# Performance work log

Hardware: AMD Instinct MI355X
Metric: run time of the kernel (lower is better)

## Reference

```python
import jax, jax.numpy as jnp
import numpy as np

B, T, D = 16, 2048, 1024


def setup_inputs() -> dict:
    key = jax.random.key(0)
    ks = jax.random.split(key, 7)
    s = 1.0 / np.sqrt(D)  # nn.Linear default init bound
    u = lambda k, shape: jax.random.uniform(k, shape, jnp.float32, -s, s)
    return {
        "x": jax.random.normal(ks[0], (B, T, D), jnp.float32),
        "h0": jnp.zeros((B, D), jnp.float32),
        "W_in": u(ks[1], (2 * D, D)),
        "b_in": u(ks[2], (2 * D,)),
        "W_dt": u(ks[3], (D, D)),
        "b_dt": u(ks[4], (D,)),
        "W_out": u(ks[5], (D, D)),
        "b_out": u(ks[6], (D,)),
    }


def reference(x, h0, W_in, b_in, W_dt, b_dt, W_out, b_out):
    # in_proj then chunk: first half x_part, second half gate
    xz = jnp.einsum("btd,ed->bte", x, W_in) + b_in          # [B,T,2D]
    x_part, gate = jnp.split(xz, 2, axis=-1)                  # each [B,T,D]
    dt = jax.nn.sigmoid(jnp.einsum("btd,ed->bte", x_part, W_dt) + b_dt)  # [B,T,D]

    def step(h, inp):
        dt_t, xp_t = inp                                      # [B,D] each
        h = (1.0 - dt_t) * h + dt_t * xp_t                    # gated EMA update
        return h, h

    _, hs = jax.lax.scan(step, h0,
                         (jnp.swapaxes(dt, 0, 1), jnp.swapaxes(x_part, 0, 1)))
    hs = jnp.swapaxes(hs, 0, 1)                               # [B,T,D]
    y = jnp.einsum("btd,ed->bte", hs * jax.nn.sigmoid(gate), W_out) + b_out
    return y
```

## Files before the change

### kernel.cpp

```cpp
#include <hip/hip_runtime.h>
#include <hip/hip_bf16.h>
#include <cstdint>

typedef __attribute__((ext_vector_type(8))) short short8;
typedef __attribute__((ext_vector_type(4))) float f32x4;
typedef __attribute__((ext_vector_type(8))) unsigned short ushort8;

#define B_ 16
#define T_ 2048
#define D_ 1024
#define M_ (B_*T_)
#define NC 32
#define CL 64

static __device__ __forceinline__ float bf2f(unsigned short u) {
  unsigned int x = ((unsigned int)u) << 16;
  return __builtin_bit_cast(float, x);
}
static __device__ __forceinline__ unsigned short f2bf(float f) {
  unsigned int x = __builtin_bit_cast(unsigned int, f);
  unsigned int r = x + 0x7fffu + ((x >> 16) & 1u);
  return (unsigned short)(r >> 16);
}
static __device__ __forceinline__ float sigmoidf(float v) {
  return 1.f / (1.f + __expf(-v));
}

typedef const __attribute__((address_space(1))) unsigned int* gas1_t;
typedef __attribute__((address_space(3))) unsigned int* las3_t;
static __device__ __forceinline__ void async_copy16(const void* g, void* l) {
  __builtin_amdgcn_global_load_lds((gas1_t)g, (las3_t)l, 16, 0, 0);
}

#define VMCNT4 asm volatile("s_waitcnt vmcnt(4)" ::: "memory")
#define VMCNT2 asm volatile("s_waitcnt vmcnt(2)" ::: "memory")
#define VMCNT0 asm volatile("s_waitcnt vmcnt(0)" ::: "memory")
#define LGKM0  asm volatile("s_waitcnt lgkmcnt(0)" ::: "memory")
#define SBAR   __builtin_amdgcn_s_barrier()
#define SCHED0 __builtin_amdgcn_sched_barrier(0)

__global__ void cvt_f32_bf16(const float* __restrict__ in,
                             unsigned short* __restrict__ out, long n8) {
  long i = (long)blockIdx.x * blockDim.x + threadIdx.x;
  long stride = (long)gridDim.x * blockDim.x;
  for (; i < n8; i += stride) {
    const float4* p = (const float4*)(in + i * 8);
    float4 a = p[0], b = p[1];
    ushort8 o;
    o[0] = f2bf(a.x); o[1] = f2bf(a.y); o[2] = f2bf(a.z); o[3] = f2bf(a.w);
    o[4] = f2bf(b.x); o[5] = f2bf(b.y); o[6] = f2bf(b.z); o[7] = f2bf(b.w);
    *(ushort8*)(out + i * 8) = o;
  }
}

__global__ void cvt_w3(const float* __restrict__ w1, unsigned short* __restrict__ o1,
                       const float* __restrict__ w2, unsigned short* __restrict__ o2,
                       const float* __restrict__ w3, unsigned short* __restrict__ o3) {
  long i = (long)blockIdx.x * blockDim.x + threadIdx.x;
  const float* src; unsigned short* dst; long off;
  if (i < 262144)      { src = w1; dst = o1; off = i; }
  else if (i < 393216) { src = w2; dst = o2; off = i - 262144; }
  else                 { src = w3; dst = o3; off = i - 393216; }
  const float4* p = (const float4*)(src + off * 8);
  float4 a = p[0], b = p[1];
  ushort8 o;
  o[0] = f2bf(a.x); o[1] = f2bf(a.y); o[2] = f2bf(a.z); o[3] = f2bf(a.w);
  o[4] = f2bf(b.x); o[5] = f2bf(b.y); o[6] = f2bf(b.z); o[7] = f2bf(b.w);
  *(ushort8*)(dst + off * 8) = o;
}

template<int EPI>
__global__ __launch_bounds__(512, 2) void gemm256(
    const unsigned short* __restrict__ A, long lda,
    const unsigned short* __restrict__ Bw,
    const float* __restrict__ bias,
    void* __restrict__ Cout, long ldc,
    int nbx)
{
  constexpr int KT = 16;
  __shared__ __align__(16) unsigned short lds[65536];

  const int tid = threadIdx.x;
  const int l  = tid & 63, w = tid >> 6;
  const int wm = w >> 2, wn = w & 3;
  const int fr = l & 15, g = l >> 4;
  const int t8 = tid >> 3;
  const int c8x = ((l & 7) ^ (l >> 3)) << 4;
  const int s0 = ((g ^ (fr & 7)) << 4);
  const int s1 = s0 ^ 0x40;
  const int tB = (w >> 2) * 64 + (w & 3) * 8 + (l >> 3);

  const int nwg = gridDim.x;
  const int cpx = nwg >> 3;
  const int bid = blockIdx.x;
  const int swz = (bid & 7) * cpx + (bid >> 3);
  const long m0 = (long)(swz / nbx) * 256;
  const long n0 = (long)(swz % nbx) * 256;

  const char* Ab = (const char*)A;
  const char* Bb = (const char*)Bw;
  const long ldab = lda * 2;
  char* LB = (char*)lds;

  auto stA = [&](int kt, int h, int nb) {
    char* lb = LB + nb * 32768 + h * 16384 + w * 1024;
    long col = (long)kt * 128 + c8x;
    async_copy16(Ab + (m0 + h * 64 + t8) * ldab + col, lb);
    async_copy16(Ab + (m0 + 128 + h * 64 + t8) * ldab + col, lb + 8192);
  };
  auto stB = [&](int kt, int h, int nb) {
    char* lb = LB + 65536 + nb * 32768 + h * 16384 + w * 1024;
    long col = (long)kt * 128 + c8x;
    async_copy16(Bb + (n0 + tB + h * 32) * 2048 + col, lb);
    async_copy16(Bb + (n0 + tB + 128 + h * 32) * 2048 + col, lb + 8192);
  };

  f32x4 acc[8][4] = {};

  stA(0, 0, 0); stB(0, 0, 0); stA(0, 1, 0); stB(0, 1, 0);
  VMCNT4; SCHED0; SBAR;

#define RD_A(DST, MH) do {                                                     \
    const char* p0_ = LB + cur * 32768 + (MH) * 16384 + wm * 8192 + fr * 128 + s0; \
    const char* p1_ = LB + cur * 32768 + (MH) * 16384 + wm * 8192 + fr * 128 + s1; \
    _Pragma("unroll") for (int mi = 0; mi < 4; ++mi) {                         \
      DST[mi][0] = *(const short8*)(p0_ + mi * 2048);                          \
      DST[mi][1] = *(const short8*)(p1_ + mi * 2048); }                        \
  } while (0)
#define RD_B(DST, NH) do {                                                     \
    const char* p0_ = LB + 65536 + cur * 32768 + (NH) * 16384 + wn * 4096 + fr * 128 + s0; \
    const char* p1_ = LB + 65536 + cur * 32768 + (NH) * 16384 + wn * 4096 + fr * 128 + s1; \
    _Pragma("unroll") for (int ni = 0; ni < 2; ++ni) {                         \
      DST[ni][0] = *(const short8*)(p0_ + ni * 2048);                          \
      DST[ni][1] = *(const short8*)(p1_ + ni * 2048); }                        \
  } while (0)
#define MM(AF, BF, MB, NB) do {                                                \
    __builtin_amdgcn_s_setprio(1);                                             \
    _Pragma("unroll") for (int mi = 0; mi < 4; ++mi)                           \
    _Pragma("unroll") for (int ni = 0; ni < 2; ++ni) {                         \
      acc[(MB)+mi][(NB)+ni] = __builtin_amdgcn_mfma_f32_16x16x32_bf16(         \
          AF[mi][0], BF[ni][0], acc[(MB)+mi][(NB)+ni], 0, 0, 0);               \
      acc[(MB)+mi][(NB)+ni] = __builtin_amdgcn_mfma_f32_16x16x32_bf16(         \
          AF[mi][1], BF[ni][1], acc[(MB)+mi][(NB)+ni], 0, 0, 0); }             \
    __builtin_amdgcn_s_setprio(0);                                             \
  } while (0)

  for (int t = 0; t < KT; ++t) {
    const int cur = t & 1, nxt = cur ^ 1;
    const bool notlast = (t + 1 < KT);
    short8 af0[4][2], af1[4][2], bf0[2][2], bf1[2][2];
    RD_A(af0, 0); RD_B(bf0, 0);
    if (notlast) stA(t + 1, 0, nxt);
    SCHED0; SBAR;
    MM(af0, bf0, 0, 0);
    if (notlast) { VMCNT4; } else { VMCNT2; }
    SCHED0; SBAR; SCHED0;
    RD_A(af1, 1);
    if (notlast) stB(t + 1, 0, nxt);
    SCHED0; SBAR;
    MM(af1, bf0, 4, 0);
    if (notlast) { VMCNT4; } else { VMCNT0; }
    SCHED0; SBAR; SCHED0;
    RD_B(bf1, 1);
    if (notlast) stA(t + 1, 1, nxt);
    SCHED0; SBAR;
    MM(af1, bf1, 4, 2);
    SCHED0; SBAR; SCHED0;
    RD_A(af0, 0);
    if (notlast) stB(t + 1, 1, nxt);
    SCHED0; SBAR;
    MM(af0, bf1, 0, 2);
    if (notlast) { VMCNT4; }
    SCHED0; SBAR; SCHED0;
  }
#undef RD_A
#undef RD_B
#undef MM

  __syncthreads();

  char* ep = LB + w * 16384;
  const int rq = l >> 4;
  if (EPI != 2) {
#pragma unroll
    for (int mi = 0; mi < 8; ++mi)
#pragma unroll
      for (int ni = 0; ni < 4; ++ni) {
        int cl = ni * 16 + fr;
        float bv = bias[n0 + wn * 64 + cl];
#pragma unroll
        for (int r = 0; r < 4; ++r) {
          float v = acc[mi][ni][r] + bv;
          if (EPI == 1) v = sigmoidf(v);
          int row = mi * 16 + rq * 4 + r;
          int byte = (row * 128 + cl * 2) ^ ((row & 7) << 4);
          *(unsigned short*)(ep + byte) = f2bf(v);
        }
      }
    LGKM0; SCHED0;
#pragma unroll
    for (int i = 0; i < 16; ++i) {
      int row = i * 8 + (l >> 3);
      int cb = (l & 7) * 16;
      int byte = (row * 128 + cb) ^ ((row & 7) << 4);
      short8 v = *(const short8*)(ep + byte);
      *(short8*)((unsigned short*)Cout + (m0 + wm * 128 + row) * ldc
                 + n0 + wn * 64 + (cb >> 1)) = v;
    }
  } else {
#pragma unroll
    for (int p = 0; p < 2; ++p) {
#pragma unroll
      for (int mi = 0; mi < 4; ++mi)
#pragma unroll
        for (int ni = 0; ni < 4; ++ni) {
          int cl = ni * 16 + fr;
          float bv = bias[n0 + wn * 64 + cl];
#pragma unroll
          for (int r = 0; r < 4; ++r) {
            float v = acc[p * 4 + mi][ni][r] + bv;
            int row = mi * 16 + rq * 4 + r;
            int byte = (row * 256 + cl * 4) ^ ((row & 7) << 4);
            *(float*)(ep + byte) = v;
          }
        }
      LGKM0; SCHED0;
#pragma unroll
      for (int i = 0; i < 16; ++i) {
        int row = i * 4 + (l >> 4);
        int cb = (l & 15) * 16;
        int byte = (row * 256 + cb) ^ ((row & 7) << 4);
        f32x4 v = *(const f32x4*)(ep + byte);
        *(f32x4*)((float*)Cout + (m0 + wm * 128 + p * 64 + row) * ldc
                  + n0 + wn * 64 + (cb >> 2)) = v;
      }
      LGKM0; SCHED0;
    }
  }
}

__global__ void scan_passA(const unsigned short* __restrict__ dtb,
                           const unsigned short* __restrict__ xz,
                           float* __restrict__ P, float* __restrict__ Hl)
{
  int idx = blockIdx.x * blockDim.x + threadIdx.x;
  int d8 = idx & 127;
  int c  = (idx >> 7) & 31;
  int b  = idx >> 12;
  int d0 = d8 * 8;
  long mbase = (long)b * T_ + (long)c * CL;
  float h[8] = {0,0,0,0,0,0,0,0};
  float p[8] = {1,1,1,1,1,1,1,1};
  for (int t = 0; t < CL; ++t) {
    long m = mbase + t;
    ushort8 dv = *(const ushort8*)(dtb + m * D_ + d0);
    ushort8 xv = *(const ushort8*)(xz + m * (2 * D_) + d0);
#pragma unroll
    for (int j = 0; j < 8; ++j) {
      float dt = bf2f(dv[j]);
      float xp = bf2f(xv[j]);
      float om = 1.f - dt;
      h[j] = om * h[j] + dt * xp;
      p[j] *= om;
    }
  }
  long pb = ((long)(b * NC + c)) * D_ + d0;
#pragma unroll
  for (int j = 0; j < 8; ++j) { P[pb + j] = p[j]; Hl[pb + j] = h[j]; }
}

__global__ void scan_passC(unsigned short* dts,
                           const unsigned short* __restrict__ xz,
                           const float* __restrict__ h0,
                           const float* __restrict__ P,
                           const float* __restrict__ Hl)
{
  int idx = blockIdx.x * blockDim.x + threadIdx.x;
  int d8 = idx & 127;
  int c  = (idx >> 7) & 31;
  int b  = idx >> 12;
  int d0 = d8 * 8;
  long mbase = (long)b * T_ + (long)c * CL;

  float h[8];
#pragma unroll
  for (int j = 0; j < 8; ++j) h[j] = h0[(long)b * D_ + d0 + j];

  for (int jc = 0; jc < c; ++jc) {
    long pb = ((long)(b * NC + jc)) * D_ + d0;
    float pj[8], hj[8];
    *(f32x4*)&pj[0] = *(const f32x4*)(P + pb);
    *(f32x4*)&pj[4] = *(const f32x4*)(P + pb + 4);
    *(f32x4*)&hj[0] = *(const f32x4*)(Hl + pb);
    *(f32x4*)&hj[4] = *(const f32x4*)(Hl + pb + 4);
#pragma unroll
    for (int j = 0; j < 8; ++j) h[j] = hj[j] + pj[j] * h[j];
  }

  for (int t = 0; t < CL; ++t) {
    long m = mbase + t;
    ushort8 dv = *(const ushort8*)(dts + m * D_ + d0);
    ushort8 xv = *(const ushort8*)(xz + m * (2 * D_) + d0);
    ushort8 gv = *(const ushort8*)(xz + m * (2 * D_) + D_ + d0);
    ushort8 ov;
#pragma unroll
    for (int j = 0; j < 8; ++j) {
      float dt = bf2f(dv[j]);
      float xp = bf2f(xv[j]);
      h[j] = (1.f - dt) * h[j] + dt * xp;
      float gt = bf2f(gv[j]);
      ov[j] = f2bf(h[j] * sigmoidf(gt));
    }
    *(ushort8*)(dts + m * D_ + d0) = ov;
  }
}

extern "C" void kernel_launch(void* const* d_in, const int* in_sizes, int n_in,
                              void* d_out, int out_size, void* d_ws, size_t ws_size,
                              hipStream_t stream) {
  const float* x     = (const float*)d_in[0];
  const float* h0    = (const float*)d_in[1];
  const float* W_in  = (const float*)d_in[2];
  const float* b_in  = (const float*)d_in[3];
  const float* W_dt  = (const float*)d_in[4];
  const float* b_dt  = (const float*)d_in[5];
  const float* W_out = (const float*)d_in[6];
  const float* b_out = (const float*)d_in[7];
  float* out = (float*)d_out;

  char* ws = (char*)d_ws;
  const size_t OFF_XB    = 0;
  const size_t OFF_WIN   = 67108864;
  const size_t OFF_WDT   = 71303168;
  const size_t OFF_WOUT  = 73400320;
  const size_t OFF_XZ    = 75497472;
  const size_t OFF_DTS   = 209715200;
  const size_t OFF_P     = 276824064;
  const size_t OFF_HL    = 278921216;
  const size_t NEEDED    = 281018368;
  if (ws_size < NEEDED) return;

  unsigned short* xb    = (unsigned short*)(ws + OFF_XB);
  unsigned short* wbin  = (unsigned short*)(ws + OFF_WIN);
  unsigned short* wbdt  = (unsigned short*)(ws + OFF_WDT);
  unsigned short* wbout = (unsigned short*)(ws + OFF_WOUT);
  unsigned short* xz    = (unsigned short*)(ws + OFF_XZ);
  unsigned short* dts   = (unsigned short*)(ws + OFF_DTS);
  float* P  = (float*)(ws + OFF_P);
  float* Hl = (float*)(ws + OFF_HL);

  cvt_f32_bf16<<<2048, 256, 0, stream>>>(x, xb, (long)M_ * D_ / 8);
  cvt_w3<<<2048, 256, 0, stream>>>(W_in, wbin, W_dt, wbdt, W_out, wbout);

  gemm256<0><<<(M_/256)*(2*D_/256), 512, 0, stream>>>(xb, D_, wbin, b_in, xz, 2*D_, 2*D_/256);
  gemm256<1><<<(M_/256)*(D_/256), 512, 0, stream>>>(xz, 2*D_, wbdt, b_dt, dts, D_, D_/256);
  scan_passA<<<256, 256, 0, stream>>>(dts, xz, P, Hl);
  scan_passC<<<256, 256, 0, stream>>>(dts, xz, h0, P, Hl);
  gemm256<2><<<(M_/256)*(D_/256), 512, 0, stream>>>(dts, D_, wbout, b_out, out, D_, D_/256);
}
```

Baseline: 446.7 us.

## Restructure GEMM main loop with register double-buffered fragments and merge convert kernels

```diff
diff --git a/kernel.cpp b/kernel.cpp
--- a/kernel.cpp
+++ b/kernel.cpp
@@ -32,41 +32,30 @@
   __builtin_amdgcn_global_load_lds((gas1_t)g, (las3_t)l, 16, 0, 0);
 }
 
-#define VMCNT4 asm volatile("s_waitcnt vmcnt(4)" ::: "memory")
-#define VMCNT2 asm volatile("s_waitcnt vmcnt(2)" ::: "memory")
 #define VMCNT0 asm volatile("s_waitcnt vmcnt(0)" ::: "memory")
 #define LGKM0  asm volatile("s_waitcnt lgkmcnt(0)" ::: "memory")
 #define SBAR   __builtin_amdgcn_s_barrier()
 #define SCHED0 __builtin_amdgcn_sched_barrier(0)
 
-__global__ void cvt_f32_bf16(const float* __restrict__ in,
-                             unsigned short* __restrict__ out, long n8) {
+__global__ void cvt_all(const float* __restrict__ x,  unsigned short* __restrict__ xb,
+                        const float* __restrict__ w1, unsigned short* __restrict__ o1,
+                        const float* __restrict__ w2, unsigned short* __restrict__ o2,
+                        const float* __restrict__ w3, unsigned short* __restrict__ o3) {
   long i = (long)blockIdx.x * blockDim.x + threadIdx.x;
   long stride = (long)gridDim.x * blockDim.x;
-  for (; i < n8; i += stride) {
-    const float4* p = (const float4*)(in + i * 8);
+  for (; i < 4718592; i += stride) {
+    const float* src; unsigned short* dst; long off;
+    if (i < 4194304)      { src = x;  dst = xb; off = i; }
+    else if (i < 4456448) { src = w1; dst = o1; off = i - 4194304; }
+    else if (i < 4587520) { src = w2; dst = o2; off = i - 4456448; }
+    else                  { src = w3; dst = o3; off = i - 4587520; }
+    const float4* p = (const float4*)(src + off * 8);
     float4 a = p[0], b = p[1];
     ushort8 o;
     o[0] = f2bf(a.x); o[1] = f2bf(a.y); o[2] = f2bf(a.z); o[3] = f2bf(a.w);
     o[4] = f2bf(b.x); o[5] = f2bf(b.y); o[6] = f2bf(b.z); o[7] = f2bf(b.w);
-    *(ushort8*)(out + i * 8) = o;
-  }
-}
-
-__global__ void cvt_w3(const float* __restrict__ w1, unsigned short* __restrict__ o1,
-                       const float* __restrict__ w2, unsigned short* __restrict__ o2,
-                       const float* __restrict__ w3, unsigned short* __restrict__ o3) {
-  long i = (long)blockIdx.x * blockDim.x + threadIdx.x;
-  const float* src; unsigned short* dst; long off;
-  if (i < 262144)      { src = w1; dst = o1; off = i; }
-  else if (i < 393216) { src = w2; dst = o2; off = i - 262144; }
-  else                 { src = w3; dst = o3; off = i - 393216; }
-  const float4* p = (const float4*)(src + off * 8);
-  float4 a = p[0], b = p[1];
-  ushort8 o;
-  o[0] = f2bf(a.x); o[1] = f2bf(a.y); o[2] = f2bf(a.z); o[3] = f2bf(a.w);
-  o[4] = f2bf(b.x); o[5] = f2bf(b.y); o[6] = f2bf(b.z); o[7] = f2bf(b.w);
-  *(ushort8*)(dst + off * 8) = o;
+    *(ushort8*)(dst + off * 8) = o;
+  }
 }
 
 template<int EPI>
@@ -116,20 +105,18 @@
   };
 
   f32x4 acc[8][4] = {};
-
-  stA(0, 0, 0); stB(0, 0, 0); stA(0, 1, 0); stB(0, 1, 0);
-  VMCNT4; SCHED0; SBAR;
-
-#define RD_A(DST, MH) do {                                                     \
-    const char* p0_ = LB + cur * 32768 + (MH) * 16384 + wm * 8192 + fr * 128 + s0; \
-    const char* p1_ = LB + cur * 32768 + (MH) * 16384 + wm * 8192 + fr * 128 + s1; \
+  short8 afX[4][2], afY[4][2], bfX[2][2], bfY[2][2];
+
+#define RD_A(DST, MH, CUR) do {                                                \
+    const char* p0_ = LB + (CUR) * 32768 + (MH) * 16384 + wm * 8192 + fr * 128 + s0; \
+    const char* p1_ = LB + (CUR) * 32768 + (MH) * 16384 + wm * 8192 + fr * 128 + s1; \
     _Pragma("unroll") for (int mi = 0; mi < 4; ++mi) {                         \
       DST[mi][0] = *(const short8*)(p0_ + mi * 2048);                          \
       DST[mi][1] = *(const short8*)(p1_ + mi * 2048); }                        \
   } while (0)
-#define RD_B(DST, NH) do {                                                     \
-    const char* p0_ = LB + 65536 + cur * 32768 + (NH) * 16384 + wn * 4096 + fr * 128 + s0; \
-    const char* p1_ = LB + 65536 + cur * 32768 + (NH) * 16384 + wn * 4096 + fr * 128 + s1; \
+#define RD_B(DST, NH, CUR) do {                                                \
+    const char* p0_ = LB + 65536 + (CUR) * 32768 + (NH) * 16384 + wn * 4096 + fr * 128 + s0; \
+    const char* p1_ = LB + 65536 + (CUR) * 32768 + (NH) * 16384 + wn * 4096 + fr * 128 + s1; \
     _Pragma("unroll") for (int ni = 0; ni < 2; ++ni) {                         \
       DST[ni][0] = *(const short8*)(p0_ + ni * 2048);                          \
       DST[ni][1] = *(const short8*)(p1_ + ni * 2048); }                        \
@@ -145,37 +132,39 @@
     __builtin_amdgcn_s_setprio(0);                                             \
   } while (0)
 
-  for (int t = 0; t < KT; ++t) {
-    const int cur = t & 1, nxt = cur ^ 1;
-    const bool notlast = (t + 1 < KT);
-    short8 af0[4][2], af1[4][2], bf0[2][2], bf1[2][2];
-    RD_A(af0, 0); RD_B(bf0, 0);
-    if (notlast) stA(t + 1, 0, nxt);
-    SCHED0; SBAR;
-    MM(af0, bf0, 0, 0);
-    if (notlast) { VMCNT4; } else { VMCNT2; }
-    SCHED0; SBAR; SCHED0;
-    RD_A(af1, 1);
-    if (notlast) stB(t + 1, 0, nxt);
-    SCHED0; SBAR;
-    MM(af1, bf0, 4, 0);
-    if (notlast) { VMCNT4; } else { VMCNT0; }
-    SCHED0; SBAR; SCHED0;
-    RD_B(bf1, 1);
-    if (notlast) stA(t + 1, 1, nxt);
-    SCHED0; SBAR;
-    MM(af1, bf1, 4, 2);
-    SCHED0; SBAR; SCHED0;
-    RD_A(af0, 0);
-    if (notlast) stB(t + 1, 1, nxt);
-    SCHED0; SBAR;
-    MM(af0, bf1, 0, 2);
-    if (notlast) { VMCNT4; }
-    SCHED0; SBAR; SCHED0;
+#define TILE(TV, CUR, AF0, AF1, BF0, BF1) do {                                 \
+    const int t_ = (TV); const bool nl = (t_ + 1 < KT);                        \
+                                                                       \
+    RD_A(AF1, 1, CUR); SCHED0;                                                 \
+    if (nl) { stA(t_ + 1, 0, (CUR) ^ 1); stB(t_ + 1, 0, (CUR) ^ 1); } SCHED0;  \
+    MM(AF0, BF0, 0, 0);                                                        \
+    SBAR; SCHED0;                                                              \
+                                                                       \
+    RD_B(BF1, 1, CUR); SCHED0;                                                 \
+    if (nl) { stA(t_ + 1, 1, (CUR) ^ 1); stB(t_ + 1, 1, (CUR) ^ 1); } SCHED0;  \
+    MM(AF1, BF0, 4, 0);                                                        \
+    SBAR; SCHED0;                                                              \
+                                                                       \
+    MM(AF1, BF1, 4, 2);                                                        \
+    VMCNT0; SCHED0; SBAR; SCHED0;                                              \
+                                                                       \
+    if (nl) { RD_A(AF1, 0, (CUR) ^ 1); RD_B(BF0, 0, (CUR) ^ 1); } SCHED0;      \
+    MM(AF0, BF1, 0, 2);                                                        \
+    SBAR; SCHED0;                                                              \
+  } while (0)
+
+  stA(0, 0, 0); stB(0, 0, 0); stA(0, 1, 0); stB(0, 1, 0);
+  VMCNT0; SCHED0; SBAR;
+  RD_A(afX, 0, 0); RD_B(bfX, 0, 0); SCHED0;
+
+  for (int t = 0; t < KT; t += 2) {
+    TILE(t,     0, afX, afY, bfX, bfY);
+    TILE(t + 1, 1, afY, afX, bfX, bfY);
   }
 #undef RD_A
 #undef RD_B
 #undef MM
+#undef TILE
 
   __syncthreads();
 
@@ -349,8 +338,7 @@
   float* P  = (float*)(ws + OFF_P);
   float* Hl = (float*)(ws + OFF_HL);
 
-  cvt_f32_bf16<<<2048, 256, 0, stream>>>(x, xb, (long)M_ * D_ / 8);
-  cvt_w3<<<2048, 256, 0, stream>>>(W_in, wbin, W_dt, wbdt, W_out, wbout);
+  cvt_all<<<2048, 256, 0, stream>>>(x, xb, W_in, wbin, W_dt, wbdt, W_out, wbout);
 
   gemm256<0><<<(M_/256)*(2*D_/256), 512, 0, stream>>>(xb, D_, wbin, b_in, xz, 2*D_, 2*D_/256);
   gemm256<1><<<(M_/256)*(D_/256), 512, 0, stream>>>(xz, 2*D_, wbdt, b_dt, dts, D_, D_/256);
```

Result: slower. 690.7 us (+54.6%).
